# Optimization experiments

Measured on AMD Instinct MI355X. Metric: run time of the kernel, lower is better.

## Reference

```python
import jax, jax.numpy as jnp
import numpy as np

LATENT = 3
POLY = 3
SINDY_DIM = 22  # 3 ones + 3 linear + 6 quad + 10 cubic


def sindy_library(z, poly_order=POLY, latent_dim=LATENT):
    # z: [N, latent_dim] -> [N, sindy_dim]; mirrors the torch loop ordering.
    N = z.shape[0]
    cols = [jnp.ones((N,), z.dtype) for _ in range(latent_dim)]
    if poly_order > 0:
        cols += [z[:, i] for i in range(latent_dim)]
    if poly_order > 1:
        for i in range(latent_dim):
            for j in range(i, latent_dim):
                cols.append(z[:, i] * z[:, j])
    if poly_order > 2:
        for i in range(latent_dim):
            for j in range(i, latent_dim):
                for k in range(j, latent_dim):
                    cols.append(z[:, i] * z[:, j] * z[:, k])
    return jnp.stack(cols, axis=1)


def _xavier(key, out_f, in_f):
    lim = np.sqrt(6.0 / (in_f + out_f)).astype(np.float32)
    return jax.random.uniform(key, (out_f, in_f), jnp.float32, -lim, lim)


def setup_inputs() -> dict:
    key = jax.random.key(0)
    ks = jax.random.split(key, 16)
    N, D = 262144, 128
    we = [128, 64, 32, 3]
    wd = [3, 32, 64, 128]
    d = {}
    d["x"] = jax.random.normal(ks[0], (N, D), jnp.float32)
    d["dx"] = jax.random.normal(ks[1], (N, D), jnp.float32)
    for li, (i_f, o_f) in enumerate(zip(we[:-1], we[1:])):
        d[f"We{li+1}"] = _xavier(ks[2 + li], o_f, i_f)
        d[f"be{li+1}"] = jnp.zeros((o_f,), jnp.float32)
    for li, (i_f, o_f) in enumerate(zip(wd[:-1], wd[1:])):
        d[f"Wd{li+1}"] = _xavier(ks[6 + li], o_f, i_f)
        d[f"bd{li+1}"] = jnp.zeros((o_f,), jnp.float32)
    d["EW"] = jnp.full((LATENT, SINDY_DIM), 0.5, jnp.float32)  # nn.init.constant_(E.weight, 0.5)
    d["Eb"] = jax.random.normal(ks[10], (LATENT,), jnp.float32) * 0.1
    return d


def reference(x, dx, We1, be1, We2, be2, We3, be3,
              Wd1, bd1, Wd2, bd2, Wd3, bd3, EW, Eb):
    # encoder forward (Linear + Identity chain)
    z = ((x @ We1.T + be1) @ We2.T + be2) @ We3.T + be3            # [N, L]
    # encoder Jacobian is constant (pure linear chain): J_enc = We3 @ We2 @ We1
    J_enc = We3 @ We2 @ We1                                        # [L, D]
    dz = dx @ J_enc.T                                              # [N, L]
    # SINDy prediction of z-dot
    theta = sindy_library(z)                                       # [N, SINDY_DIM]
    dzb = theta @ EW.T + Eb                                        # [N, L]
    # decoder forward
    xb = ((z @ Wd1.T + bd1) @ Wd2.T + bd2) @ Wd3.T + bd3           # [N, D]
    # decoder Jacobian (constant)
    J_dec = Wd3 @ Wd2 @ Wd1                                        # [D, L]
    dxb = dzb @ J_dec.T                                            # [N, D]
    return z, dz, dzb, xb, dxb
```

## Files before the change

### kernel.cpp

```cpp
#include <hip/hip_runtime.h>

#define D 128
#define RPB 128

typedef float f32x4 __attribute__((ext_vector_type(4)));

__device__ __forceinline__ float dpp_half_sum(float v) {
    #define DPP_STEP(ctrl, rowmask)                                           \
        v += __int_as_float(__builtin_amdgcn_update_dpp(                      \
                 0, __float_as_int(v), (ctrl), (rowmask), 0xF, true))
    DPP_STEP(0x111, 0xF);
    DPP_STEP(0x112, 0xF);
    DPP_STEP(0x114, 0xF);
    DPP_STEP(0x118, 0xF);
    DPP_STEP(0x142, 0xA);
    #undef DPP_STEP
    return v;
}

__global__ __launch_bounds__(256) void fuse_weights(
    const float* __restrict__ We1, const float* __restrict__ be1,
    const float* __restrict__ We2, const float* __restrict__ be2,
    const float* __restrict__ We3, const float* __restrict__ be3,
    const float* __restrict__ Wd1, const float* __restrict__ bd1,
    const float* __restrict__ Wd2, const float* __restrict__ bd2,
    const float* __restrict__ Wd3, const float* __restrict__ bd3,
    float* __restrict__ ws)
{
    __shared__ float A1[3][64];
    __shared__ float B1[64][3];
    __shared__ float t2d[64];
    const int t = threadIdx.x;

    if (t < 192) {
        {   int r = t >> 6, c = t & 63;
            float s = 0.f;
            #pragma unroll 8
            for (int i = 0; i < 32; ++i) s += We3[r * 32 + i] * We2[i * 64 + c];
            A1[r][c] = s;
        }
        {   int o = t / 3, l = t - o * 3;
            float s = 0.f;
            #pragma unroll 8
            for (int i = 0; i < 32; ++i) s += Wd2[o * 32 + i] * Wd1[i * 3 + l];
            B1[o][l] = s;
        }
    } else {
        int i = t - 192;
        float s = bd2[i];
        #pragma unroll 8
        for (int j = 0; j < 32; ++j) s += Wd2[i * 32 + j] * bd1[j];
        t2d[i] = s;
    }
    __syncthreads();

    for (int e = t; e < 3 * D; e += 256) {
        int r = e >> 7, c = e & 127;
        float s = 0.f;
        #pragma unroll 8
        for (int j = 0; j < 64; ++j) s += A1[r][j] * We1[j * D + c];
        ws[e] = s;
    }
    if (t < 3) {
        float s = be3[t];
        #pragma unroll 8
        for (int j = 0; j < 64; ++j) s += A1[t][j] * be1[j];
        #pragma unroll 8
        for (int i = 0; i < 32; ++i) s += We3[t * 32 + i] * be2[i];
        ws[384 + t] = s;
    }
    if (t < 128) {
        float s0 = 0.f, s1 = 0.f, s2 = 0.f, sb = bd3[t];
        #pragma unroll 8
        for (int j = 0; j < 64; ++j) {
            float w = Wd3[t * 64 + j];
            s0 += w * B1[j][0];
            s1 += w * B1[j][1];
            s2 += w * B1[j][2];
            sb += w * t2d[j];
        }
        ws[512 + t * 4 + 0] = s0;
        ws[512 + t * 4 + 1] = s1;
        ws[512 + t * 4 + 2] = s2;
        ws[512 + t * 4 + 3] = sb;
    }
}

__global__ __launch_bounds__(256) void sindy_all(
    const float* __restrict__ x, const float* __restrict__ dx,
    const float* __restrict__ EW, const float* __restrict__ Eb,
    const float* __restrict__ ws, float* __restrict__ out, int nrows)
{
    __shared__ alignas(16) float sz[RPB * 3];
    __shared__ alignas(16) float sdz[RPB * 3];
    __shared__ alignas(16) float sdzb[RPB * 3];
    __shared__ alignas(16) float sew[69];

    const int t    = threadIdx.x;
    const int lane = t & 31;
    const int half = t >> 5;

    if (t < 69) sew[t] = (t < 66) ? EW[t] : Eb[t - 66];

    const f32x4 je0 = *((const f32x4*)(ws +   0) + lane);
    const f32x4 je1 = *((const f32x4*)(ws + 128) + lane);
    const f32x4 je2 = *((const f32x4*)(ws + 256) + lane);
    const float benc0 = ws[384], benc1 = ws[385], benc2 = ws[386];
    const f32x4 jd0 = *((const f32x4*)(ws + 512) + lane * 4 + 0);
    const f32x4 jd1 = *((const f32x4*)(ws + 512) + lane * 4 + 1);
    const f32x4 jd2 = *((const f32x4*)(ws + 512) + lane * 4 + 2);
    const f32x4 jd3 = *((const f32x4*)(ws + 512) + lane * 4 + 3);

    const int base = blockIdx.x * RPB;
    const int rem  = nrows - base;

    #pragma unroll 4
    for (int i = 0; i < RPB / 8; ++i) {
        const int r2  = i * 8 + half;
        const int row = base + r2;
        if (row >= nrows) continue;
        const f32x4 xv = ((const f32x4*)(x + (size_t)row * D))[lane];
        float z0 = je0.x*xv.x + je0.y*xv.y + je0.z*xv.z + je0.w*xv.w;
        float z1 = je1.x*xv.x + je1.y*xv.y + je1.z*xv.z + je1.w*xv.w;
        float z2 = je2.x*xv.x + je2.y*xv.y + je2.z*xv.z + je2.w*xv.w;
        z0 = dpp_half_sum(z0);
        z1 = dpp_half_sum(z1);
        z2 = dpp_half_sum(z2);
        if (lane == 31) {
            sz[r2 * 3 + 0] = z0 + benc0;
            sz[r2 * 3 + 1] = z1 + benc1;
            sz[r2 * 3 + 2] = z2 + benc2;
        }
    }

    #pragma unroll 4
    for (int i = 0; i < RPB / 8; ++i) {
        const int r2  = i * 8 + half;
        const int row = base + r2;
        if (row >= nrows) continue;
        const f32x4 dv = ((const f32x4*)(dx + (size_t)row * D))[lane];
        float d0 = je0.x*dv.x + je0.y*dv.y + je0.z*dv.z + je0.w*dv.w;
        float d1 = je1.x*dv.x + je1.y*dv.y + je1.z*dv.z + je1.w*dv.w;
        float d2 = je2.x*dv.x + je2.y*dv.y + je2.z*dv.z + je2.w*dv.w;
        d0 = dpp_half_sum(d0);
        d1 = dpp_half_sum(d1);
        d2 = dpp_half_sum(d2);
        if (lane == 31) {
            sdz[r2 * 3 + 0] = d0;
            sdz[r2 * 3 + 1] = d1;
            sdz[r2 * 3 + 2] = d2;
        }
    }

    __syncthreads();

    if (t < RPB && t < rem) {
        const float z0 = sz[t * 3 + 0];
        const float z1 = sz[t * 3 + 1];
        const float z2 = sz[t * 3 + 2];

        const float q00 = z0*z0, q01 = z0*z1, q02 = z0*z2;
        const float q11 = z1*z1, q12 = z1*z2, q22 = z2*z2;
        float th[19];
        th[0]=z0;  th[1]=z1;  th[2]=z2;
        th[3]=q00; th[4]=q01; th[5]=q02; th[6]=q11; th[7]=q12; th[8]=q22;
        th[9]=q00*z0;  th[10]=q00*z1; th[11]=q00*z2;
        th[12]=q11*z0; th[13]=q12*z0; th[14]=q22*z0;
        th[15]=q11*z1; th[16]=q11*z2; th[17]=q22*z1; th[18]=q22*z2;

        float b0 = sew[66] + sew[0]  + sew[1]  + sew[2];
        float b1 = sew[67] + sew[22] + sew[23] + sew[24];
        float b2 = sew[68] + sew[44] + sew[45] + sew[46];
        #pragma unroll
        for (int k = 0; k < 19; ++k) {
            b0 += sew[3  + k] * th[k];
            b1 += sew[25 + k] * th[k];
            b2 += sew[47 + k] * th[k];
        }
        sdzb[t * 3 + 0] = b0;
        sdzb[t * 3 + 1] = b1;
        sdzb[t * 3 + 2] = b2;
    }

    __syncthreads();

    if (rem >= RPB) {
        if (t < RPB * 3 / 4) {
            __builtin_nontemporal_store(((const f32x4*)sz)[t],
                (f32x4*)(out + (size_t)base * 3) + t);
            __builtin_nontemporal_store(((const f32x4*)sdz)[t],
                (f32x4*)(out + 3 * (size_t)nrows + (size_t)base * 3) + t);
            __builtin_nontemporal_store(((const f32x4*)sdzb)[t],
                (f32x4*)(out + 6 * (size_t)nrows + (size_t)base * 3) + t);
        }
    } else {
        for (int e = t; e < rem * 3; e += 256) {
            out[(size_t)base * 3 + e]                     = sz[e];
            out[3 * (size_t)nrows + (size_t)base * 3 + e] = sdz[e];
            out[6 * (size_t)nrows + (size_t)base * 3 + e] = sdzb[e];
        }
    }

    float* __restrict__ xbout = out + 9 * (size_t)nrows;
    #pragma unroll 4
    for (int i = 0; i < RPB / 8; ++i) {
        const int r2  = i * 8 + half;
        const int row = base + r2;
        if (row >= nrows) continue;
        const float z0 = sz[r2 * 3 + 0];
        const float z1 = sz[r2 * 3 + 1];
        const float z2 = sz[r2 * 3 + 2];
        f32x4 v;
        v.x = jd0.x*z0 + jd0.y*z1 + jd0.z*z2 + jd0.w;
        v.y = jd1.x*z0 + jd1.y*z1 + jd1.z*z2 + jd1.w;
        v.z = jd2.x*z0 + jd2.y*z1 + jd2.z*z2 + jd2.w;
        v.w = jd3.x*z0 + jd3.y*z1 + jd3.z*z2 + jd3.w;
        __builtin_nontemporal_store(v, (f32x4*)(xbout + (size_t)row * D) + lane);
    }

    float* __restrict__ dxbout = out + 137 * (size_t)nrows;
    #pragma unroll 4
    for (int i = 0; i < RPB / 8; ++i) {
        const int r2  = i * 8 + half;
        const int row = base + r2;
        if (row >= nrows) continue;
        const float b0 = sdzb[r2 * 3 + 0];
        const float b1 = sdzb[r2 * 3 + 1];
        const float b2 = sdzb[r2 * 3 + 2];
        f32x4 v;
        v.x = jd0.x*b0 + jd0.y*b1 + jd0.z*b2;
        v.y = jd1.x*b0 + jd1.y*b1 + jd1.z*b2;
        v.z = jd2.x*b0 + jd2.y*b1 + jd2.z*b2;
        v.w = jd3.x*b0 + jd3.y*b1 + jd3.z*b2;
        __builtin_nontemporal_store(v, (f32x4*)(dxbout + (size_t)row * D) + lane);
    }
}

extern "C" void kernel_launch(void* const* d_in, const int* in_sizes, int n_in,
                              void* d_out, int out_size, void* d_ws, size_t ws_size,
                              hipStream_t stream) {
    const float* x   = (const float*)d_in[0];
    const float* dx  = (const float*)d_in[1];
    const float* We1 = (const float*)d_in[2];
    const float* be1 = (const float*)d_in[3];
    const float* We2 = (const float*)d_in[4];
    const float* be2 = (const float*)d_in[5];
    const float* We3 = (const float*)d_in[6];
    const float* be3 = (const float*)d_in[7];
    const float* Wd1 = (const float*)d_in[8];
    const float* bd1 = (const float*)d_in[9];
    const float* Wd2 = (const float*)d_in[10];
    const float* bd2 = (const float*)d_in[11];
    const float* Wd3 = (const float*)d_in[12];
    const float* bd3 = (const float*)d_in[13];
    const float* EW  = (const float*)d_in[14];
    const float* Eb  = (const float*)d_in[15];

    float* ws  = (float*)d_ws;
    float* out = (float*)d_out;
    const int nrows = in_sizes[0] / D;
    const int nblk  = (nrows + RPB - 1) / RPB;

    fuse_weights<<<1, 256, 0, stream>>>(We1, be1, We2, be2, We3, be3,
                                        Wd1, bd1, Wd2, bd2, Wd3, bd3, ws);

    sindy_all<<<nblk, 256, 0, stream>>>(x, dx, EW, Eb, ws, out, nrows);
}
```

Measured before the change: 109.1 us.

## Split fused kernel into separate encoder and decoder kernels

Splits the single fused kernel into an encoder kernel, which reads x and dx and writes z, dz and dzb, and a decoder kernel, which reads z and dzb back from the output and writes xb and dxb. Each phase then has its own kernel with lower register and shared memory pressure, so a phase can stream at full bandwidth instead of alternating read-heavy and write-heavy phases within one block. It also switches the small output stores from nontemporal to ordinary stores, so the decoder can likely reread them from cache. The cost is an extra launch and an extra round trip of z and dzb through memory.

Result: slower. 122.7 us (+12.5%).

```diff
diff --git a/kernel.cpp b/kernel.cpp
--- a/kernel.cpp
+++ b/kernel.cpp
@@ -86,7 +86,7 @@
     }
 }
 
-__global__ __launch_bounds__(256) void sindy_all(
+__global__ __launch_bounds__(256) void enc_k(
     const float* __restrict__ x, const float* __restrict__ dx,
     const float* __restrict__ EW, const float* __restrict__ Eb,
     const float* __restrict__ ws, float* __restrict__ out, int nrows)
@@ -106,10 +106,6 @@
     const f32x4 je1 = *((const f32x4*)(ws + 128) + lane);
     const f32x4 je2 = *((const f32x4*)(ws + 256) + lane);
     const float benc0 = ws[384], benc1 = ws[385], benc2 = ws[386];
-    const f32x4 jd0 = *((const f32x4*)(ws + 512) + lane * 4 + 0);
-    const f32x4 jd1 = *((const f32x4*)(ws + 512) + lane * 4 + 1);
-    const f32x4 jd2 = *((const f32x4*)(ws + 512) + lane * 4 + 2);
-    const f32x4 jd3 = *((const f32x4*)(ws + 512) + lane * 4 + 3);
 
     const int base = blockIdx.x * RPB;
     const int rem  = nrows - base;
@@ -186,12 +182,9 @@
 
     if (rem >= RPB) {
         if (t < RPB * 3 / 4) {
-            __builtin_nontemporal_store(((const f32x4*)sz)[t],
-                (f32x4*)(out + (size_t)base * 3) + t);
-            __builtin_nontemporal_store(((const f32x4*)sdz)[t],
-                (f32x4*)(out + 3 * (size_t)nrows + (size_t)base * 3) + t);
-            __builtin_nontemporal_store(((const f32x4*)sdzb)[t],
-                (f32x4*)(out + 6 * (size_t)nrows + (size_t)base * 3) + t);
+            ((f32x4*)(out + (size_t)base * 3))[t]                     = ((const f32x4*)sz)[t];
+            ((f32x4*)(out + 3 * (size_t)nrows + (size_t)base * 3))[t] = ((const f32x4*)sdz)[t];
+            ((f32x4*)(out + 6 * (size_t)nrows + (size_t)base * 3))[t] = ((const f32x4*)sdzb)[t];
         }
     } else {
         for (int e = t; e < rem * 3; e += 256) {
@@ -200,6 +193,39 @@
             out[6 * (size_t)nrows + (size_t)base * 3 + e] = sdzb[e];
         }
     }
+}
+
+__global__ __launch_bounds__(256) void dec_k(
+    const float* __restrict__ ws, const float* __restrict__ out_ro,
+    float* __restrict__ out, int nrows)
+{
+    __shared__ alignas(16) float sz[RPB * 3];
+    __shared__ alignas(16) float sdzb[RPB * 3];
+
+    const int t    = threadIdx.x;
+    const int lane = t & 31;
+    const int half = t >> 5;
+
+    const f32x4 jd0 = *((const f32x4*)(ws + 512) + lane * 4 + 0);
+    const f32x4 jd1 = *((const f32x4*)(ws + 512) + lane * 4 + 1);
+    const f32x4 jd2 = *((const f32x4*)(ws + 512) + lane * 4 + 2);
+    const f32x4 jd3 = *((const f32x4*)(ws + 512) + lane * 4 + 3);
+
+    const int base = blockIdx.x * RPB;
+    const int rem  = nrows - base;
+
+    if (rem >= RPB) {
+        if (t < RPB * 3 / 4) {
+            ((f32x4*)sz)[t]   = ((const f32x4*)(out_ro + (size_t)base * 3))[t];
+            ((f32x4*)sdzb)[t] = ((const f32x4*)(out_ro + 6 * (size_t)nrows + (size_t)base * 3))[t];
+        }
+    } else {
+        for (int e = t; e < rem * 3; e += 256) {
+            sz[e]   = out_ro[(size_t)base * 3 + e];
+            sdzb[e] = out_ro[6 * (size_t)nrows + (size_t)base * 3 + e];
+        }
+    }
+    __syncthreads();
 
     float* __restrict__ xbout = out + 9 * (size_t)nrows;
     #pragma unroll 4
@@ -264,5 +290,7 @@
     fuse_weights<<<1, 256, 0, stream>>>(We1, be1, We2, be2, We3, be3,
                                         Wd1, bd1, Wd2, bd2, Wd3, bd3, ws);
 
-    sindy_all<<<nblk, 256, 0, stream>>>(x, dx, EW, Eb, ws, out, nrows);
-}
+    enc_k<<<nblk, 256, 0, stream>>>(x, dx, EW, Eb, ws, out, nrows);
+
+    dec_k<<<nblk, 256, 0, stream>>>(ws, out, out, nrows);
+}
```
